# Optimization experiments

Hardware: AMD Instinct MI355X
Metric: run time of the kernel (lower is better)

Reference implementation:

```python
import jax, jax.numpy as jnp
import numpy as np

DIM = 1024
NUM_HEADS = 16


def setup_inputs() -> dict:
    key = jax.random.key(0)
    ks = jax.random.split(key, 5)
    x = jax.random.normal(ks[0], (2, 2048, DIM), dtype=jnp.float32)
    s = 1.0 / np.sqrt(DIM)
    W_qkv = jax.random.normal(ks[1], (DIM, 3 * DIM), dtype=jnp.float32) * s
    b_qkv = jax.random.normal(ks[2], (3 * DIM,), dtype=jnp.float32) * 0.01
    W_proj = jax.random.normal(ks[3], (DIM, DIM), dtype=jnp.float32) * s
    b_proj = jax.random.normal(ks[4], (DIM,), dtype=jnp.float32) * 0.01
    return {"x": x, "W_qkv": W_qkv, "b_qkv": b_qkv, "W_proj": W_proj, "b_proj": b_proj}


def reference(x, W_qkv, b_qkv, W_proj, b_proj):
    B, T, C = x.shape
    H = NUM_HEADS
    D = C // H  # head dim
    qkv = x @ W_qkv + b_qkv                      # (B,T,3C)
    q, k, v = jnp.split(qkv, 3, axis=-1)
    # (B,T,C) -> (B,H,T,D)
    q = q.reshape(B, T, H, D).transpose(0, 2, 1, 3)
    k = k.reshape(B, T, H, D).transpose(0, 2, 1, 3)
    v = v.reshape(B, T, H, D).transpose(0, 2, 1, 3)
    att = jnp.einsum('bhqd,bhkd->bhqk', q, k) * (1.0 / np.sqrt(D))
    causal = jnp.tril(jnp.ones((T, T), dtype=bool))
    att = jnp.where(causal, att, -jnp.inf)
    att = jax.nn.softmax(att, axis=-1)
    y = jnp.einsum('bhqk,bhkd->bhqd', att, v)    # (B,H,T,D)
    y = y.transpose(0, 2, 1, 3).reshape(B, T, C)
    return y @ W_proj + b_proj
```

## Files before the change

kernel.cpp:

```cpp
#include <hip/hip_runtime.h>
#include <math.h>

#define DIM 1024
#define HEADS 16
#define HDIM 64
#define SEQ 2048
#define BATCH 2

typedef __attribute__((ext_vector_type(8))) short short8;
typedef __attribute__((ext_vector_type(4))) float f32x4;

__device__ __forceinline__ unsigned short bf16_rtn(float x) {
    union { float f; unsigned int u; } c; c.f = x;
    unsigned int r = c.u + 0x7fffu + ((c.u >> 16) & 1u);
    return (unsigned short)(r >> 16);
}
__device__ __forceinline__ float bf16_to_f(unsigned short h) {
    union { unsigned int u; float f; } c; c.u = ((unsigned int)h) << 16;
    return c.f;
}
__device__ __forceinline__ void split_bf16(float x, unsigned short& hi, unsigned short& lo) {
    hi = bf16_rtn(x);
    lo = bf16_rtn(x - bf16_to_f(hi));
}

__global__ __launch_bounds__(256) void prep_a_kernel(
    const float* __restrict__ A, unsigned short* __restrict__ Ah,
    unsigned short* __restrict__ Al, int K)
{
    const int mu = blockIdx.x;
    const int nku = K >> 5;
    const int t = threadIdx.x;
    const int c = t & 15;
    const int pb = t >> 4;
    const int npairs = K >> 3;
    for (int p = pb; p < npairs; p += 16) {
        const int ku = p >> 2, g = p & 3;
        const float* src = A + (size_t)(mu * 16 + c) * K + ku * 32 + g * 8;
        const float4 f0 = ((const float4*)src)[0];
        const float4 f1 = ((const float4*)src)[1];
        const float tf[8] = {f0.x, f0.y, f0.z, f0.w, f1.x, f1.y, f1.z, f1.w};
        unsigned int hw[4], lw[4];
#pragma unroll
        for (int j = 0; j < 4; ++j) {
            unsigned short h0, l0, h1, l1;
            split_bf16(tf[2 * j], h0, l0);
            split_bf16(tf[2 * j + 1], h1, l1);
            hw[j] = (unsigned int)h0 | ((unsigned int)h1 << 16);
            lw[j] = (unsigned int)l0 | ((unsigned int)l1 << 16);
        }
        const size_t off = ((size_t)mu * nku + ku) * 512 + g * 128 + c * 8;
        *(uint4*)(Ah + off) = *(uint4*)hw;
        *(uint4*)(Al + off) = *(uint4*)lw;
    }
}

__global__ __launch_bounds__(256) void prep_w_kernel(
    const float* __restrict__ W, unsigned short* __restrict__ Wh,
    unsigned short* __restrict__ Wl, int K, int N)
{
    const int nu = blockIdx.x;
    const int nku = K >> 5;
    const int t = threadIdx.x;
    const int c = t & 15;
    const int pb = t >> 4;
    const int npairs = K >> 3;
    for (int p = pb; p < npairs; p += 16) {
        const int ku = p >> 2, g = p & 3;
        unsigned int hw[4], lw[4];
#pragma unroll
        for (int j = 0; j < 4; ++j) {
            const float v0 = W[(size_t)(ku * 32 + g * 8 + 2 * j) * N + nu * 16 + c];
            const float v1 = W[(size_t)(ku * 32 + g * 8 + 2 * j + 1) * N + nu * 16 + c];
            unsigned short h0, l0, h1, l1;
            split_bf16(v0, h0, l0);
            split_bf16(v1, h1, l1);
            hw[j] = (unsigned int)h0 | ((unsigned int)h1 << 16);
            lw[j] = (unsigned int)l0 | ((unsigned int)l1 << 16);
        }
        const size_t off = ((size_t)nu * nku + ku) * 512 + g * 128 + c * 8;
        *(uint4*)(Wh + off) = *(uint4*)hw;
        *(uint4*)(Wl + off) = *(uint4*)lw;
    }
}

__global__ __launch_bounds__(256) void gemm_frag(
    const unsigned short* __restrict__ Ah, const unsigned short* __restrict__ Al,
    const unsigned short* __restrict__ Bh, const unsigned short* __restrict__ Bl,
    const float* __restrict__ bias, float* __restrict__ C,
    int M, int N, int K)
{
    __shared__ __align__(16) unsigned short sm[16384];
    const int nku = K >> 5;
    const int tid = threadIdx.x;
    const int w = tid >> 6, lane = tid & 63;
    const int c = lane & 15, g = lane >> 4;
    const int bm = blockIdx.y * 128, bn = blockIdx.x * 128;
    const int wm = (w >> 1) * 64, wn = (w & 1) * 64;

    const unsigned short* srcp[8];
    int dsto[8];
#pragma unroll
    for (int i = 0; i < 8; ++i) {
        const int flat = i * 256 + tid;
        const int luid = flat >> 6, gran = flat & 63;
        const int buf = luid >> 3, uloc = luid & 7;
        const unsigned short* base = (buf == 0) ? Ah : (buf == 1) ? Al : (buf == 2) ? Bh : Bl;
        const int rb = (buf < 2) ? bm : bn;
        srcp[i] = base + ((size_t)(rb / 16 + uloc) * nku) * 512 + gran * 8;
        dsto[i] = flat * 8;
    }

    f32x4 acc[4][4];
#pragma unroll
    for (int i = 0; i < 4; ++i)
#pragma unroll
        for (int j = 0; j < 4; ++j) acc[i][j] = (f32x4){0.f, 0.f, 0.f, 0.f};

    short8 nxt[8];
#pragma unroll
    for (int i = 0; i < 8; ++i) nxt[i] = *(const short8*)(srcp[i]);

    for (int ks = 0; ks < nku; ++ks) {
        __syncthreads();
#pragma unroll
        for (int i = 0; i < 8; ++i) *(short8*)(sm + dsto[i]) = nxt[i];
        __syncthreads();

        if (ks + 1 < nku) {
            const int off = (ks + 1) * 512;
#pragma unroll
            for (int i = 0; i < 8; ++i) nxt[i] = *(const short8*)(srcp[i] + off);
        }

        short8 ahf[4], alf[4], bhf[4], blf[4];
        const int lo = lane * 8;
#pragma unroll
        for (int f = 0; f < 4; ++f) {
            ahf[f] = *(const short8*)(sm + (wm / 16 + f) * 512 + lo);
            alf[f] = *(const short8*)(sm + (8 + wm / 16 + f) * 512 + lo);
            bhf[f] = *(const short8*)(sm + (16 + wn / 16 + f) * 512 + lo);
            blf[f] = *(const short8*)(sm + (24 + wn / 16 + f) * 512 + lo);
        }
#pragma unroll
        for (int fm = 0; fm < 4; ++fm)
#pragma unroll
            for (int fn = 0; fn < 4; ++fn) {
                f32x4 cc = acc[fm][fn];
                cc = __builtin_amdgcn_mfma_f32_16x16x32_bf16(bhf[fn], ahf[fm], cc, 0, 0, 0);
                cc = __builtin_amdgcn_mfma_f32_16x16x32_bf16(blf[fn], ahf[fm], cc, 0, 0, 0);
                cc = __builtin_amdgcn_mfma_f32_16x16x32_bf16(bhf[fn], alf[fm], cc, 0, 0, 0);
                acc[fm][fn] = cc;
            }
    }

    float4 bv[4];
#pragma unroll
    for (int fn = 0; fn < 4; ++fn)
        bv[fn] = *(const float4*)&bias[bn + wn + fn * 16 + 4 * g];
#pragma unroll
    for (int fm = 0; fm < 4; ++fm) {
        const int row = bm + wm + fm * 16 + c;
        float* cp = C + (size_t)row * N + bn + wn + 4 * g;
#pragma unroll
        for (int fn = 0; fn < 4; ++fn) {
            float4 o;
            o.x = acc[fm][fn][0] + bv[fn].x;
            o.y = acc[fm][fn][1] + bv[fn].y;
            o.z = acc[fm][fn][2] + bv[fn].z;
            o.w = acc[fm][fn][3] + bv[fn].w;
            *(float4*)(cp + fn * 16) = o;
        }
    }
}

__global__ __launch_bounds__(256) void attn_mfma_kernel(
    const float* __restrict__ qkv, float* __restrict__ y)
{
    __shared__ __align__(16) char smem[49152];
    unsigned short* Kh = (unsigned short*)smem;
    unsigned short* Kl = (unsigned short*)(smem + 8192);
    unsigned short* Vh = (unsigned short*)(smem + 16384);
    unsigned short* Vl = (unsigned short*)(smem + 24576);

    const int tid = threadIdx.x;
    const int w = tid >> 6, lane = tid & 63;
    const int c = lane & 15;
    const int g = lane >> 4;
    const int C3 = 3 * DIM;

    const int tilemax = (int)gridDim.x - 1;
    const int tile = blockIdx.z ? (int)blockIdx.x : (tilemax - (int)blockIdx.x);
    const int qb = tile * 128;
    const int h = blockIdx.y, b = blockIdx.z;
    const int qw = qb + 32 * w;

    char* Pw = (w < 2) ? (smem + 8192 * w) : (smem + 32768 + 8192 * (w - 2));
    unsigned short* Ph = (unsigned short*)Pw;
    unsigned short* Pl = (unsigned short*)(Pw + 4096);

    const float* base = qkv + (size_t)b * SEQ * C3;

    short8 q_hi[2][2], q_lo[2][2];
#pragma unroll
    for (int nf = 0; nf < 2; ++nf)
#pragma unroll
        for (int kf = 0; kf < 2; ++kf) {
            const int row = qw + 16 * nf + c;
            const int d0 = 32 * kf + 8 * g;
            const float4* qp = (const float4*)(base + (size_t)row * C3 + h * HDIM + d0);
            float4 f0 = qp[0], f1 = qp[1];
            float tf[8] = {f0.x, f0.y, f0.z, f0.w, f1.x, f1.y, f1.z, f1.w};
#pragma unroll
            for (int j = 0; j < 8; ++j) {
                unsigned short hh, ll;
                split_bf16(tf[j] * 0.125f, hh, ll);
                q_hi[nf][kf][j] = (short)hh;
                q_lo[nf][kf][j] = (short)ll;
            }
        }

    f32x4 o[2][4];
#pragma unroll
    for (int i = 0; i < 2; ++i)
#pragma unroll
        for (int j = 0; j < 4; ++j) o[i][j] = (f32x4){0.f, 0.f, 0.f, 0.f};
    float m_run[2] = {-3.0e30f, -3.0e30f};
    float l_run[2] = {0.f, 0.f};

    const int nch = qb / 64 + 2;
    for (int ch = 0; ch < nch; ++ch) {
        const int kb = ch * 64;
        __syncthreads();

#pragma unroll
        for (int i = 0; i < 2; ++i) {
            const int s = tid + 256 * i;
            const int sc = s & 15, sg = (s >> 4) & 3, skf = (s >> 6) & 1, smf = s >> 7;
            const int row = kb + 16 * smf + sc;
            const int d0 = 32 * skf + 8 * sg;
            const float4* kp = (const float4*)(base + (size_t)row * C3 + DIM + h * HDIM + d0);
            float4 f0 = kp[0], f1 = kp[1];
            float tf[8] = {f0.x, f0.y, f0.z, f0.w, f1.x, f1.y, f1.z, f1.w};
            unsigned int hw[4], lw[4];
#pragma unroll
            for (int j = 0; j < 4; ++j) {
                unsigned short h0, l0, h1, l1;
                split_bf16(tf[2 * j], h0, l0);
                split_bf16(tf[2 * j + 1], h1, l1);
                hw[j] = (unsigned int)h0 | ((unsigned int)h1 << 16);
                lw[j] = (unsigned int)l0 | ((unsigned int)l1 << 16);
            }
            *(uint4*)((char*)Kh + s * 16) = *(uint4*)hw;
            *(uint4*)((char*)Kl + s * 16) = *(uint4*)lw;
        }
#pragma unroll
        for (int i = 0; i < 2; ++i) {
            const int s2 = tid + 256 * i;
            const int rp = s2 >> 4, c4 = s2 & 15;
            const float* r0 = base + (size_t)(kb + 2 * rp) * C3 + 2 * DIM + h * HDIM + 4 * c4;
            const float* r1 = r0 + C3;
            float4 a = *(const float4*)r0;
            float4 bq = *(const float4*)r1;
            const float* af = (const float*)&a;
            const float* bf = (const float*)&bq;
            const int kf = rp >> 4, gg = (rp >> 2) & 3, joff = 4 * (rp & 3);
#pragma unroll
            for (int ii = 0; ii < 4; ++ii) {
                const int d = 4 * c4 + ii;
                const int slot = (((d >> 4) * 2 + kf) * 4 + gg) * 16 + (d & 15);
                unsigned short h0, l0, h1, l1;
                split_bf16(af[ii], h0, l0);
                split_bf16(bf[ii], h1, l1);
                *(unsigned int*)((char*)Vh + slot * 16 + joff) = (unsigned int)h0 | ((unsigned int)h1 << 16);
                *(unsigned int*)((char*)Vl + slot * 16 + joff) = (unsigned int)l0 | ((unsigned int)l1 << 16);
            }
        }
        __syncthreads();

        const bool active = (kb <= qw + 31);
        const bool diag = active && (kb + 63 > qw);
        f32x4 st[4][2];
        float fscale[2];

        if (active) {
#pragma unroll
            for (int mf = 0; mf < 4; ++mf)
#pragma unroll
                for (int nf = 0; nf < 2; ++nf) st[mf][nf] = (f32x4){0.f, 0.f, 0.f, 0.f};
#pragma unroll
            for (int kf = 0; kf < 2; ++kf)
#pragma unroll
                for (int mf = 0; mf < 4; ++mf) {
                    const int slot = ((mf * 2 + kf) * 4 + g) * 16 + c;
                    short8 ah = *(const short8*)((const char*)Kh + slot * 16);
                    short8 al = *(const short8*)((const char*)Kl + slot * 16);
#pragma unroll
                    for (int nf = 0; nf < 2; ++nf) {
                        st[mf][nf] = __builtin_amdgcn_mfma_f32_16x16x32_bf16(ah, q_hi[nf][kf], st[mf][nf], 0, 0, 0);
                        st[mf][nf] = __builtin_amdgcn_mfma_f32_16x16x32_bf16(ah, q_lo[nf][kf], st[mf][nf], 0, 0, 0);
                        st[mf][nf] = __builtin_amdgcn_mfma_f32_16x16x32_bf16(al, q_hi[nf][kf], st[mf][nf], 0, 0, 0);
                    }
                }
#pragma unroll
            for (int nf = 0; nf < 2; ++nf) {
                float cm = -3.0e30f;
#pragma unroll
                for (int mf = 0; mf < 4; ++mf)
#pragma unroll
                    for (int r = 0; r < 4; ++r) {
                        float s = st[mf][nf][r];
                        if (diag && (kb + 16 * mf + 4 * g + r > qw + 16 * nf + c)) s = -3.0e30f;
                        st[mf][nf][r] = s;
                        cm = fmaxf(cm, s);
                    }
                cm = fmaxf(cm, __shfl_xor(cm, 16));
                cm = fmaxf(cm, __shfl_xor(cm, 32));
                const float mnew = fmaxf(m_run[nf], cm);
                fscale[nf] = __expf(m_run[nf] - mnew);
                m_run[nf] = mnew;
                l_run[nf] *= fscale[nf];
            }
#pragma unroll
            for (int mf = 0; mf < 2; ++mf) {
                const float fo = fscale[mf];
#pragma unroll
                for (int nf = 0; nf < 4; ++nf) {
                    o[mf][nf][0] *= fo; o[mf][nf][1] *= fo;
                    o[mf][nf][2] *= fo; o[mf][nf][3] *= fo;
                }
            }
        }
        __syncthreads();

        if (active) {
#pragma unroll
            for (int nf = 0; nf < 2; ++nf) {
#pragma unroll
                for (int mf = 0; mf < 4; ++mf) {
                    const int slot = ((nf * 2 + (mf >> 1)) * 4 + ((2 * mf + (g >> 1)) & 3)) * 16 + c;
                    const int bofs = slot * 16 + 8 * (g & 1);
#pragma unroll
                    for (int k = 0; k < 2; ++k) {
                        const float p0 = __expf(st[mf][nf][2 * k] - m_run[nf]);
                        const float p1 = __expf(st[mf][nf][2 * k + 1] - m_run[nf]);
                        l_run[nf] += p0 + p1;
                        unsigned short h0, l0, h1, l1;
                        split_bf16(p0, h0, l0);
                        split_bf16(p1, h1, l1);
                        *(unsigned int*)((char*)Ph + bofs + 4 * k) = (unsigned int)h0 | ((unsigned int)h1 << 16);
                        *(unsigned int*)((char*)Pl + bofs + 4 * k) = (unsigned int)l0 | ((unsigned int)l1 << 16);
                    }
                }
            }
#pragma unroll
            for (int kf = 0; kf < 2; ++kf) {
                short8 pa_h[2], pa_l[2];
#pragma unroll
                for (int mf = 0; mf < 2; ++mf) {
                    const int slot = ((mf * 2 + kf) * 4 + g) * 16 + c;
                    pa_h[mf] = *(const short8*)((const char*)Ph + slot * 16);
                    pa_l[mf] = *(const short8*)((const char*)Pl + slot * 16);
                }
#pragma unroll
                for (int nf = 0; nf < 4; ++nf) {
                    const int slot = ((nf * 2 + kf) * 4 + g) * 16 + c;
                    short8 vb_h = *(const short8*)((const char*)Vh + slot * 16);
                    short8 vb_l = *(const short8*)((const char*)Vl + slot * 16);
#pragma unroll
                    for (int mf = 0; mf < 2; ++mf) {
                        o[mf][nf] = __builtin_amdgcn_mfma_f32_16x16x32_bf16(vb_h, pa_h[mf], o[mf][nf], 0, 0, 0);
                        o[mf][nf] = __builtin_amdgcn_mfma_f32_16x16x32_bf16(vb_l, pa_h[mf], o[mf][nf], 0, 0, 0);
                        o[mf][nf] = __builtin_amdgcn_mfma_f32_16x16x32_bf16(vb_h, pa_l[mf], o[mf][nf], 0, 0, 0);
                    }
                }
            }
        }
    }

    float linv[2];
#pragma unroll
    for (int nf = 0; nf < 2; ++nf) {
        float lt = l_run[nf];
        lt += __shfl_xor(lt, 16);
        lt += __shfl_xor(lt, 32);
        linv[nf] = 1.0f / lt;
    }
#pragma unroll
    for (int mf = 0; mf < 2; ++mf) {
        const float li = linv[mf];
        const int row = qw + 16 * mf + c;
        float* yp = y + ((size_t)b * SEQ + row) * DIM + h * HDIM + 4 * g;
#pragma unroll
        for (int nf = 0; nf < 4; ++nf) {
            float4 ov;
            ov.x = o[mf][nf][0] * li;
            ov.y = o[mf][nf][1] * li;
            ov.z = o[mf][nf][2] * li;
            ov.w = o[mf][nf][3] * li;
            *(float4*)(yp + 16 * nf) = ov;
        }
    }
}

extern "C" void kernel_launch(void* const* d_in, const int* in_sizes, int n_in,
                              void* d_out, int out_size, void* d_ws, size_t ws_size,
                              hipStream_t stream)
{
    const float* x      = (const float*)d_in[0];
    const float* W_qkv  = (const float*)d_in[1];
    const float* b_qkv  = (const float*)d_in[2];
    const float* W_proj = (const float*)d_in[3];
    const float* b_proj = (const float*)d_in[4];
    float* out = (float*)d_out;

    char* ws = (char*)d_ws;
    float* qkv          = (float*)(ws);
    float* y            = (float*)(ws + 50331648);
    unsigned short* Xh  = (unsigned short*)(ws + 67108864);
    unsigned short* Xl  = (unsigned short*)(ws + 75497472);
    unsigned short* Wqh = (unsigned short*)(ws + 83886080);
    unsigned short* Wql = (unsigned short*)(ws + 90177536);
    unsigned short* Wph = (unsigned short*)(ws + 96468992);
    unsigned short* Wpl = (unsigned short*)(ws + 98566144);

    const int M = BATCH * SEQ;

    prep_w_kernel<<<3 * DIM / 16, 256, 0, stream>>>(W_qkv, Wqh, Wql, DIM, 3 * DIM);
    prep_w_kernel<<<DIM / 16, 256, 0, stream>>>(W_proj, Wph, Wpl, DIM, DIM);
    prep_a_kernel<<<M / 16, 256, 0, stream>>>(x, Xh, Xl, DIM);

    gemm_frag<<<dim3(3 * DIM / 128, M / 128), 256, 0, stream>>>(
        Xh, Xl, Wqh, Wql, b_qkv, qkv, M, 3 * DIM, DIM);

    attn_mfma_kernel<<<dim3(SEQ / 128, HEADS, BATCH), 256, 0, stream>>>(qkv, y);

    prep_a_kernel<<<M / 16, 256, 0, stream>>>(y, Xh, Xl, DIM);
    gemm_frag<<<dim3(DIM / 128, M / 128), 256, 0, stream>>>(
        Xh, Xl, Wph, Wpl, b_proj, out, M, DIM, DIM);
}
```

Measured before the change: 348.7 us.

## Pre-split K/V into fragment layout and emit attention output as bf16 fragments

A new prep kernel converts K and V once per chunk into hi/lo bf16 MFMA-fragment layout. Attention then copies those tiles straight into LDS, prefetching the next chunk into registers instead of re-splitting fp32 K/V in every query-tile block. The attention epilogue writes Y directly in the split fragment layout, so the separate prep_a pass before the output projection is dropped. The softmax scale is folded with log2(e) so exp2f can be used. The QKV GEMM now writes Q and KV to separate buffers. This trades an extra kernel and workspace aliasing for less redundant conversion work and less fp32 traffic.

```diff
diff --git a/kernel.cpp b/kernel.cpp
--- a/kernel.cpp
+++ b/kernel.cpp
@@ -84,10 +84,67 @@
     }
 }
 
+__global__ __launch_bounds__(256) void prep_kv_kernel(
+    const float* __restrict__ KV,
+    unsigned short* __restrict__ Kfh, unsigned short* __restrict__ Kfl,
+    unsigned short* __restrict__ Vfh, unsigned short* __restrict__ Vfl)
+{
+    const int ch = blockIdx.x, h = blockIdx.y, b = blockIdx.z;
+    const int kb = ch * 64;
+    const int t = threadIdx.x;
+    const size_t obase = ((size_t)((b * HEADS + h) * 32 + ch)) * 4096;
+    const float* base = KV + (size_t)b * SEQ * 2048;
+
+#pragma unroll
+    for (int i = 0; i < 2; ++i) {
+        const int s = t + 256 * i;
+        const int sc = s & 15, sg = (s >> 4) & 3, skf = (s >> 6) & 1, smf = s >> 7;
+        const int row = kb + 16 * smf + sc;
+        const int d0 = 32 * skf + 8 * sg;
+        const float4* kp = (const float4*)(base + (size_t)row * 2048 + h * HDIM + d0);
+        const float4 f0 = kp[0], f1 = kp[1];
+        const float tf[8] = {f0.x, f0.y, f0.z, f0.w, f1.x, f1.y, f1.z, f1.w};
+        unsigned int hw[4], lw[4];
+#pragma unroll
+        for (int j = 0; j < 4; ++j) {
+            unsigned short h0, l0, h1, l1;
+            split_bf16(tf[2 * j], h0, l0);
+            split_bf16(tf[2 * j + 1], h1, l1);
+            hw[j] = (unsigned int)h0 | ((unsigned int)h1 << 16);
+            lw[j] = (unsigned int)l0 | ((unsigned int)l1 << 16);
+        }
+        *(uint4*)(Kfh + obase + s * 8) = *(uint4*)hw;
+        *(uint4*)(Kfl + obase + s * 8) = *(uint4*)lw;
+    }
+#pragma unroll
+    for (int i = 0; i < 2; ++i) {
+        const int s = t + 256 * i;
+        const int c = s & 15, g = (s >> 4) & 3, kf = (s >> 6) & 1, nf = s >> 7;
+        const int dim = 16 * nf + c;
+        const float* vp = base + (size_t)(kb + 32 * kf + 8 * g) * 2048 + 1024 + h * HDIM + dim;
+        float tf[8];
+#pragma unroll
+        for (int e = 0; e < 8; ++e) tf[e] = vp[(size_t)e * 2048];
+        unsigned int hw[4], lw[4];
+#pragma unroll
+        for (int j = 0; j < 4; ++j) {
+            unsigned short h0, l0, h1, l1;
+            split_bf16(tf[2 * j], h0, l0);
+            split_bf16(tf[2 * j + 1], h1, l1);
+            hw[j] = (unsigned int)h0 | ((unsigned int)h1 << 16);
+            lw[j] = (unsigned int)l0 | ((unsigned int)l1 << 16);
+        }
+        *(uint4*)(Vfh + obase + s * 8) = *(uint4*)hw;
+        *(uint4*)(Vfl + obase + s * 8) = *(uint4*)lw;
+    }
+}
+
 __global__ __launch_bounds__(256) void gemm_frag(
     const unsigned short* __restrict__ Ah, const unsigned short* __restrict__ Al,
     const unsigned short* __restrict__ Bh, const unsigned short* __restrict__ Bl,
-    const float* __restrict__ bias, float* __restrict__ C,
+    const float* __restrict__ bias,
+    float* __restrict__ Cq, int ldq,
+    float* __restrict__ Ckv, int ldkv, int qsplit,
     int M, int N, int K)
 {
     __shared__ __align__(16) unsigned short sm[16384];
@@ -154,14 +211,19 @@
             }
     }
 
+    const int gc0 = bn + wn;
+    float* cbase; int ldc, ccol;
+    if (gc0 < qsplit) { cbase = Cq; ldc = ldq; ccol = gc0; }
+    else { cbase = Ckv; ldc = ldkv; ccol = gc0 - qsplit; }
+
     float4 bv[4];
 #pragma unroll
     for (int fn = 0; fn < 4; ++fn)
-        bv[fn] = *(const float4*)&bias[bn + wn + fn * 16 + 4 * g];
+        bv[fn] = *(const float4*)&bias[gc0 + fn * 16 + 4 * g];
 #pragma unroll
     for (int fm = 0; fm < 4; ++fm) {
         const int row = bm + wm + fm * 16 + c;
-        float* cp = C + (size_t)row * N + bn + wn + 4 * g;
+        float* cp = cbase + (size_t)row * ldc + ccol + 4 * g;
 #pragma unroll
         for (int fn = 0; fn < 4; ++fn) {
             float4 o;
@@ -175,7 +237,10 @@
 }
 
 __global__ __launch_bounds__(256) void attn_mfma_kernel(
-    const float* __restrict__ qkv, float* __restrict__ y)
+    const float* __restrict__ Q,
+    const unsigned short* __restrict__ Kfh, const unsigned short* __restrict__ Kfl,
+    const unsigned short* __restrict__ Vfh, const unsigned short* __restrict__ Vfl,
+    unsigned short* __restrict__ Yfh, unsigned short* __restrict__ Yfl)
 {
     __shared__ __align__(16) char smem[49152];
     unsigned short* Kh = (unsigned short*)smem;
@@ -187,7 +252,6 @@
     const int w = tid >> 6, lane = tid & 63;
     const int c = lane & 15;
     const int g = lane >> 4;
-    const int C3 = 3 * DIM;
 
     const int tilemax = (int)gridDim.x - 1;
     const int tile = blockIdx.z ? (int)blockIdx.x : (tilemax - (int)blockIdx.x);
@@ -199,7 +263,7 @@
     unsigned short* Ph = (unsigned short*)Pw;
     unsigned short* Pl = (unsigned short*)(Pw + 4096);
 
-    const float* base = qkv + (size_t)b * SEQ * C3;
+    const float QS = 0.125f * 1.44269504088896341f;
 
     short8 q_hi[2][2], q_lo[2][2];
 #pragma unroll
@@ -208,13 +272,13 @@
         for (int kf = 0; kf < 2; ++kf) {
             const int row = qw + 16 * nf + c;
             const int d0 = 32 * kf + 8 * g;
-            const float4* qp = (const float4*)(base + (size_t)row * C3 + h * HDIM + d0);
+            const float4* qp = (const float4*)(Q + ((size_t)b * SEQ + row) * DIM + h * HDIM + d0);
             float4 f0 = qp[0], f1 = qp[1];
             float tf[8] = {f0.x, f0.y, f0.z, f0.w, f1.x, f1.y, f1.z, f1.w};
 #pragma unroll
             for (int j = 0; j < 8; ++j) {
                 unsigned short hh, ll;
-                split_bf16(tf[j] * 0.125f, hh, ll);
+                split_bf16(tf[j] * QS, hh, ll);
                 q_hi[nf][kf][j] = (short)hh;
                 q_lo[nf][kf][j] = (short)ll;
             }
@@ -228,55 +292,47 @@
     float m_run[2] = {-3.0e30f, -3.0e30f};
     float l_run[2] = {0.f, 0.f};
 
+    const size_t fbase = ((size_t)(b * HEADS + h)) * (32 * 4096);
     const int nch = qb / 64 + 2;
+
+    short8 nxt[8];
+    {
+        const size_t cb = fbase;
+        nxt[0] = *(const short8*)(Kfh + cb + (size_t)tid * 8);
+        nxt[1] = *(const short8*)(Kfh + cb + (size_t)(tid + 256) * 8);
+        nxt[2] = *(const short8*)(Kfl + cb + (size_t)tid * 8);
+        nxt[3] = *(const short8*)(Kfl + cb + (size_t)(tid + 256) * 8);
+        nxt[4] = *(const short8*)(Vfh + cb + (size_t)tid * 8);
+        nxt[5] = *(const short8*)(Vfh + cb + (size_t)(tid + 256) * 8);
+        nxt[6] = *(const short8*)(Vfl + cb + (size_t)tid * 8);
+        nxt[7] = *(const short8*)(Vfl + cb + (size_t)(tid + 256) * 8);
+    }
+
     for (int ch = 0; ch < nch; ++ch) {
         const int kb = ch * 64;
         __syncthreads();
 
-#pragma unroll
-        for (int i = 0; i < 2; ++i) {
-            const int s = tid + 256 * i;
-            const int sc = s & 15, sg = (s >> 4) & 3, skf = (s >> 6) & 1, smf = s >> 7;
-            const int row = kb + 16 * smf + sc;
-            const int d0 = 32 * skf + 8 * sg;
-            const float4* kp = (const float4*)(base + (size_t)row * C3 + DIM + h * HDIM + d0);
-            float4 f0 = kp[0], f1 = kp[1];
-            float tf[8] = {f0.x, f0.y, f0.z, f0.w, f1.x, f1.y, f1.z, f1.w};
-            unsigned int hw[4], lw[4];
-#pragma unroll
-            for (int j = 0; j < 4; ++j) {
-                unsigned short h0, l0, h1, l1;
-                split_bf16(tf[2 * j], h0, l0);
-                split_bf16(tf[2 * j + 1], h1, l1);
-                hw[j] = (unsigned int)h0 | ((unsigned int)h1 << 16);
-                lw[j] = (unsigned int)l0 | ((unsigned int)l1 << 16);
-            }
-            *(uint4*)((char*)Kh + s * 16) = *(uint4*)hw;
-            *(uint4*)((char*)Kl + s * 16) = *(uint4*)lw;
-        }
-#pragma unroll
-        for (int i = 0; i < 2; ++i) {
-            const int s2 = tid + 256 * i;
-            const int rp = s2 >> 4, c4 = s2 & 15;
-            const float* r0 = base + (size_t)(kb + 2 * rp) * C3 + 2 * DIM + h * HDIM + 4 * c4;
-            const float* r1 = r0 + C3;
-            float4 a = *(const float4*)r0;
-            float4 bq = *(const float4*)r1;
-            const float* af = (const float*)&a;
-            const float* bf = (const float*)&bq;
-            const int kf = rp >> 4, gg = (rp >> 2) & 3, joff = 4 * (rp & 3);
-#pragma unroll
-            for (int ii = 0; ii < 4; ++ii) {
-                const int d = 4 * c4 + ii;
-                const int slot = (((d >> 4) * 2 + kf) * 4 + gg) * 16 + (d & 15);
-                unsigned short h0, l0, h1, l1;
-                split_bf16(af[ii], h0, l0);
-                split_bf16(bf[ii], h1, l1);
-                *(unsigned int*)((char*)Vh + slot * 16 + joff) = (unsigned int)h0 | ((unsigned int)h1 << 16);
-                *(unsigned int*)((char*)Vl + slot * 16 + joff) = (unsigned int)l0 | ((unsigned int)l1 << 16);
-            }
-        }
+        *(short8*)((char*)Kh + tid * 16) = nxt[0];
+        *(short8*)((char*)Kh + (tid + 256) * 16) = nxt[1];
+        *(short8*)((char*)Kl + tid * 16) = nxt[2];
+        *(short8*)((char*)Kl + (tid + 256) * 16) = nxt[3];
+        *(short8*)((char*)Vh + tid * 16) = nxt[4];
+        *(short8*)((char*)Vh + (tid + 256) * 16) = nxt[5];
+        *(short8*)((char*)Vl + tid * 16) = nxt[6];
+        *(short8*)((char*)Vl + (tid + 256) * 16) = nxt[7];
         __syncthreads();
+
+        if (ch + 1 < nch) {
+            const size_t cb = fbase + (size_t)(ch + 1) * 4096;
+            nxt[0] = *(const short8*)(Kfh + cb + (size_t)tid * 8);
+            nxt[1] = *(const short8*)(Kfh + cb + (size_t)(tid + 256) * 8);
+            nxt[2] = *(const short8*)(Kfl + cb + (size_t)tid * 8);
+            nxt[3] = *(const short8*)(Kfl + cb + (size_t)(tid + 256) * 8);
+            nxt[4] = *(const short8*)(Vfh + cb + (size_t)tid * 8);
+            nxt[5] = *(const short8*)(Vfh + cb + (size_t)(tid + 256) * 8);
+            nxt[6] = *(const short8*)(Vfl + cb + (size_t)tid * 8);
+            nxt[7] = *(const short8*)(Vfl + cb + (size_t)(tid + 256) * 8);
+        }
 
         const bool active = (kb <= qw + 31);
         const bool diag = active && (kb + 63 > qw);
@@ -317,7 +373,7 @@
                 cm = fmaxf(cm, __shfl_xor(cm, 16));
                 cm = fmaxf(cm, __shfl_xor(cm, 32));
                 const float mnew = fmaxf(m_run[nf], cm);
-                fscale[nf] = __expf(m_run[nf] - mnew);
+                fscale[nf] = exp2f(m_run[nf] - mnew);
                 m_run[nf] = mnew;
                 l_run[nf] *= fscale[nf];
             }
@@ -342,8 +398,8 @@
                     const int bofs = slot * 16 + 8 * (g & 1);
 #pragma unroll
                     for (int k = 0; k < 2; ++k) {
-                        const float p0 = __expf(st[mf][nf][2 * k] - m_run[nf]);
-                        const float p1 = __expf(st[mf][nf][2 * k + 1] - m_run[nf]);
+                        const float p0 = exp2f(st[mf][nf][2 * k] - m_run[nf]);
+                        const float p1 = exp2f(st[mf][nf][2 * k + 1] - m_run[nf]);
                         l_run[nf] += p0 + p1;
                         unsigned short h0, l0, h1, l1;
                         split_bf16(p0, h0, l0);
@@ -389,16 +445,26 @@
 #pragma unroll
     for (int mf = 0; mf < 2; ++mf) {
         const float li = linv[mf];
-        const int row = qw + 16 * mf + c;
-        float* yp = y + ((size_t)b * SEQ + row) * DIM + h * HDIM + 4 * g;
+        const int mu = (b * SEQ + qw + 16 * mf) >> 4;
 #pragma unroll
         for (int nf = 0; nf < 4; ++nf) {
-            float4 ov;
-            ov.x = o[mf][nf][0] * li;
-            ov.y = o[mf][nf][1] * li;
-            ov.z = o[mf][nf][2] * li;
-            ov.w = o[mf][nf][3] * li;
-            *(float4*)(yp + 16 * nf) = ov;
+            const int D0 = h * HDIM + 16 * nf + 4 * g;
+            const int ku = D0 >> 5;
+            const int gp = (D0 >> 3) & 3;
+            const int e0 = D0 & 7;
+            const size_t off = ((size_t)mu * 32 + ku) * 512 + (gp * 16 + c) * 8 + e0;
+            unsigned short h0, l0, h1, l1, h2, l2, h3, l3;
+            split_bf16(o[mf][nf][0] * li, h0, l0);
+            split_bf16(o[mf][nf][1] * li, h1, l1);
+            split_bf16(o[mf][nf][2] * li, h2, l2);
+            split_bf16(o[mf][nf][3] * li, h3, l3);
+            uint2 hy, ly;
+            hy.x = (unsigned int)h0 | ((unsigned int)h1 << 16);
+            hy.y = (unsigned int)h2 | ((unsigned int)h3 << 16);
+            ly.x = (unsigned int)l0 | ((unsigned int)l1 << 16);
+            ly.y = (unsigned int)l2 | ((unsigned int)l3 << 16);
+            *(uint2*)(Yfh + off) = hy;
+            *(uint2*)(Yfl + off) = ly;
         }
     }
 }
@@ -415,14 +481,20 @@
     float* out = (float*)d_out;
 
     char* ws = (char*)d_ws;
-    float* qkv          = (float*)(ws);
-    float* y            = (float*)(ws + 50331648);
-    unsigned short* Xh  = (unsigned short*)(ws + 67108864);
-    unsigned short* Xl  = (unsigned short*)(ws + 75497472);
-    unsigned short* Wqh = (unsigned short*)(ws + 83886080);
-    unsigned short* Wql = (unsigned short*)(ws + 90177536);
-    unsigned short* Wph = (unsigned short*)(ws + 96468992);
-    unsigned short* Wpl = (unsigned short*)(ws + 98566144);
+    float* Qbuf  = (float*)(ws);
+    float* KVbuf = (float*)(ws + 16777216);
+    unsigned short* Yfh = (unsigned short*)(ws + 16777216);
+    unsigned short* Yfl = (unsigned short*)(ws + 25165824);
+    unsigned short* Wqh = (unsigned short*)(ws + 50331648);
+    unsigned short* Wql = (unsigned short*)(ws + 56623104);
+    unsigned short* Xh  = (unsigned short*)(ws + 62914560);
+    unsigned short* Xl  = (unsigned short*)(ws + 71303168);
+    unsigned short* Kfh = (unsigned short*)(ws + 50331648);
+    unsigned short* Kfl = (unsigned short*)(ws + 58720256);
+    unsigned short* Vfh = (unsigned short*)(ws + 67108864);
+    unsigned short* Vfl = (unsigned short*)(ws + 75497472);
+    unsigned short* Wph = (unsigned short*)(ws + 83886080);
+    unsigned short* Wpl = (unsigned short*)(ws + 85983232);
 
     const int M = BATCH * SEQ;
 
@@ -431,11 +503,13 @@
     prep_a_kernel<<<M / 16, 256, 0, stream>>>(x, Xh, Xl, DIM);
 
     gemm_frag<<<dim3(3 * DIM / 128, M / 128), 256, 0, stream>>>(
-        Xh, Xl, Wqh, Wql, b_qkv, qkv, M, 3 * DIM, DIM);
-
-    attn_mfma_kernel<<<dim3(SEQ / 128, HEADS, BATCH), 256, 0, stream>>>(qkv, y);
-
-    prep_a_kernel<<<M / 16, 256, 0, stream>>>(y, Xh, Xl, DIM);
+        Xh, Xl, Wqh, Wql, b_qkv, Qbuf, DIM, KVbuf, 2048, 1024, M, 3 * DIM, DIM);
+
+    prep_kv_kernel<<<dim3(SEQ / 64, HEADS, BATCH), 256, 0, stream>>>(
+        KVbuf, Kfh, Kfl, Vfh, Vfl);
+    attn_mfma_kernel<<<dim3(SEQ / 128, HEADS, BATCH), 256, 0, stream>>>(
+        Qbuf, Kfh, Kfl, Vfh, Vfl, Yfh, Yfl);
+
     gemm_frag<<<dim3(DIM / 128, M / 128), 256, 0, stream>>>(
-        Xh, Xl, Wph, Wpl, b_proj, out, M, DIM, DIM);
-}
+        Yfh, Yfl, Wph, Wpl, b_proj, out, DIM, out, DIM, DIM, M, DIM, DIM);
+}
```

Result: faster. 329.3 us (-5.6%).
